# Performance work log

Hardware: AMD Instinct MI355X
Metric: run time of the kernel (lower is better)

The kernel has to match this reference:

```python
import jax, jax.numpy as jnp
import numpy as np
from jax import lax

B, TS, NN, FC = 16, 16, 4096, 1
HIDDEN = 64


def setup_inputs() -> dict:
    key = jax.random.key(0)
    k1, k2, k3, k4, k5 = jax.random.split(key, 5)
    x = jax.random.normal(k1, (B, TS, NN, FC), dtype=jnp.float32)
    # Conv2d(in_ch + hidden -> 4*hidden, kernel=3, padding=1), OIHW layout
    conv_w = jax.random.normal(k2, (4 * HIDDEN, FC + HIDDEN, 3, 3), dtype=jnp.float32) * 0.05
    conv_b = jax.random.normal(k3, (4 * HIDDEN,), dtype=jnp.float32) * 0.05
    # fc: Conv2d(hidden -> 1, kernel=1)
    fc_w = jax.random.normal(k4, (1, HIDDEN, 1, 1), dtype=jnp.float32) * 0.05
    fc_b = jax.random.normal(k5, (1,), dtype=jnp.float32) * 0.05
    return {"x": x, "conv_w": conv_w, "conv_b": conv_b, "fc_w": fc_w, "fc_b": fc_b}


def _convlstm_forward(x, conv_w, conv_b, fc_w, fc_b):
    Bb, Ts, Nn, Fc = x.shape
    hidden = fc_w.shape[1]
    # [B, Ts, Fc, Nn, 1] -> scan over time axis: [Ts, B, Fc, Nn, 1]
    xp = jnp.transpose(x, (0, 1, 3, 2))[..., None]
    xs = jnp.swapaxes(xp, 0, 1)
    h0 = jnp.zeros((Bb, hidden, Nn, 1), dtype=x.dtype)
    c0 = jnp.zeros_like(h0)

    dn = lax.conv_dimension_numbers(h0.shape[:1] + (Fc + hidden, Nn, 1), conv_w.shape, ("NCHW", "OIHW", "NCHW"))

    def step(carry, xt):
        h, c = carry
        inp = jnp.concatenate([xt, h], axis=1)  # [B, Fc+hidden, Nn, 1]
        gates = lax.conv_general_dilated(inp, conv_w, (1, 1), ((1, 1), (1, 1)), dimension_numbers=dn)
        gates = gates + conv_b[None, :, None, None]
        i, f, o, g = jnp.split(gates, 4, axis=1)
        c2 = jax.nn.sigmoid(f) * c + jax.nn.sigmoid(i) * jnp.tanh(g)
        h2 = jax.nn.sigmoid(o) * jnp.tanh(c2)
        return (h2, c2), None

    (h, c), _ = lax.scan(step, (h0, c0), xs)
    # fc: 1x1 conv -> [B, 1, Nn, 1]
    out = jnp.einsum("bchw,oc->bohw", h, fc_w[:, :, 0, 0]) + fc_b[None, :, None, None]
    out = out[..., 0]                 # [B, 1, Nn]
    out = jnp.transpose(out, (0, 2, 1))[:, None]  # [B, 1, Nn, 1]
    return jnp.broadcast_to(out, (Bb, Ts, Nn, 1))


def reference(x, conv_w, conv_b, fc_w, fc_b):
    return _convlstm_forward(x, conv_w, conv_b, fc_w, fc_b)
```

## Files before the change

kernel.cpp:

```cpp
#include <hip/hip_runtime.h>

typedef _Float16 f16;
typedef __attribute__((ext_vector_type(8))) _Float16 half8;
typedef __attribute__((ext_vector_type(4))) float floatx4;

#define BB    16
#define TSN   16
#define NNP   4096
#define HID   64
#define KPK   224
#define WOUT  128
#define HALO  8
#define WCMP  144
#define HROWS 146
#define NMS   9
#define NTIL  32

#define LOG2E 1.44269504088896340736f

__device__ __forceinline__ int hadr(int rr, int c) {
    return rr * 64 + ((c ^ (rr & 7)) << 3);
}
__device__ __forceinline__ unsigned f16pair(float a, float b) {
    union { f16 h; unsigned short u; } ua, ub;
    ua.h = (f16)a; ub.h = (f16)b;
    return (unsigned)ua.u | ((unsigned)ub.u << 16);
}
__device__ __forceinline__ unsigned pkrtz(float a, float b) {
    typedef __fp16 h2v __attribute__((ext_vector_type(2)));
    h2v r = __builtin_amdgcn_cvt_pkrtz(a, b);
    union { h2v h; unsigned u; } cv; cv.h = r; return cv.u;
}

__device__ __forceinline__ float fast_exp2(float x) {
#if __has_builtin(__builtin_amdgcn_exp2f)
    return __builtin_amdgcn_exp2f(x);
#else
    return exp2f(x);
#endif
}
__device__ __forceinline__ float fast_rcp(float x) {
#if __has_builtin(__builtin_amdgcn_rcpf)
    return __builtin_amdgcn_rcpf(x);
#else
    return 1.0f / x;
#endif
}

__device__ __forceinline__ float dpp_xor8(float v) {
    return __int_as_float(__builtin_amdgcn_mov_dpp(__float_as_int(v), 0x128, 0xF, 0xF, true));
}
__device__ __forceinline__ float dpp_xor1(float v) {
    return __int_as_float(__builtin_amdgcn_mov_dpp(__float_as_int(v), 0xB1, 0xF, 0xF, true));
}

__global__ void pack_w_kernel(const float* __restrict__ conv_w,
                              const float* __restrict__ conv_b,
                              f16* __restrict__ wpack) {
    int idx = blockIdx.x * 256 + threadIdx.x;
    if (idx >= 4 * 64 * KPK) return;
    int k  = idx % KPK;
    int oc = idx / KPK;
    int kt = k >> 5, c = k & 31;
    float w = 0.0f;
    if (kt < 6) {
        int tap = kt >> 1;
        int j   = (kt & 1) * 32 + c;
        w = conv_w[((oc * 65 + 1 + j) * 3 + tap) * 3 + 1];
    } else if (c < 3) {
        w = conv_w[((oc * 65 + 0) * 3 + c) * 3 + 1];
    } else if (c == 3) {
        w = conv_b[oc];
    }
    float scale = (oc >= 192) ? (2.0f * LOG2E) : (-LOG2E);
    wpack[oc * KPK + k] = (f16)(w * scale);
}

template <int MS>
__device__ __forceinline__ void do_mfma(
    const f16* __restrict__ hrd, const f16* __restrict__ xts,
    const half8 (&bf)[7][2], const floatx4& zacc,
    floatx4 (&acc)[2], int m, int kg)
{
    const int ar = MS * 16 + m;
    {
        half8 a = *(const half8*)(xts + ar * 8);
        acc[0] = __builtin_amdgcn_mfma_f32_16x16x32_f16(a, bf[6][0], zacc, 0, 0, 0);
        acc[1] = __builtin_amdgcn_mfma_f32_16x16x32_f16(a, bf[6][1], zacc, 0, 0, 0);
    }
#pragma unroll
    for (int kt = 0; kt < 6; ++kt) {
        half8 a = *(const half8*)(hrd + hadr(ar + (kt >> 1), (kt & 1) * 4 + kg));
        acc[0] = __builtin_amdgcn_mfma_f32_16x16x32_f16(a, bf[kt][0], acc[0], 0, 0, 0);
        acc[1] = __builtin_amdgcn_mfma_f32_16x16x32_f16(a, bf[kt][1], acc[1], 0, 0, 0);
    }
}

template <int MS>
__device__ __forceinline__ void do_epi(
    f16* __restrict__ hwr, floatx4 (&acc)[2], float (&creg)[NMS * 2],
    int m, int kg, int wave, bool lowm, bool edge, int n0)
{
    float pg[2][2];
#pragma unroll
    for (int q = 0; q < 2; ++q)
#pragma unroll
        for (int j = 0; j < 2; ++j) {
            float send = lowm ? acc[q][2 + j] : acc[q][j];
            pg[q][j] = dpp_xor8(send);
        }

#pragma unroll
    for (int j = 0; j < 2; ++j) {
        int r  = lowm ? j : 2 + j;
        float yi = lowm ? acc[0][j] : pg[0][j];
        float yf = lowm ? pg[0][j] : acc[0][2 + j];
        float yo = lowm ? acc[1][j] : pg[1][j];
        float yg = lowm ? pg[1][j] : acc[1][2 + j];
        float Ei = fast_exp2(yi);
        float Ef = fast_exp2(yf);
        float Eo = fast_exp2(yo);
        float Eg = fast_exp2(yg);
        float Fi = 1.0f + Ei, Ff = 1.0f + Ef, Fo = 1.0f + Eo, Fg = 1.0f + Eg;
        const int ridx = MS * 2 + j;
        float P  = Fi * Fg;
        float N  = fmaf(Eg - 1.0f, Ff, creg[ridx] * P);
        float cn = N * fast_rcp(P * Ff);
        float Ec = fast_exp2(cn * (2.0f * LOG2E));
        float hnf = (Ec - 1.0f) * fast_rcp(Fo * (1.0f + Ec));
        creg[ridx] = cn;
        int rit = MS * 16 + kg * 4 + r;
        if (edge) {
            int pos = n0 - HALO + rit;
            if (pos < 0 || pos >= NNP) hnf = 0.0f;
        }
        float po = dpp_xor1(hnf);
        if (!(m & 1)) {
            int rr = rit + 1;
            ((unsigned*)hwr)[rr * 32 + ((wave ^ (rr & 7)) << 2) + ((m & 7) >> 1)] =
                pkrtz(hnf, po);
        }
    }
}

__global__ __launch_bounds__(512, 2)
void lstm_kernel(const float* __restrict__ x, const f16* __restrict__ wpack,
                 f16* __restrict__ h_glob, float* __restrict__ c_glob, int phase)
{
    __shared__ __align__(16) f16 hlds[2][HROWS * 64];
    __shared__ __align__(16) f16 xt[8 * WCMP * 8];

    const int blk  = blockIdx.x;
    const int b    = blk >> 5;
    const int tau  = blk & 31;
    const int n0   = tau * WOUT;
    const int tid  = threadIdx.x;
    const int lane = tid & 63;
    const int wave = tid >> 6;
    const int m    = lane & 15;
    const int kg   = lane >> 4;
    const int gh   = m >> 3;
    const int hid  = wave * 8 + (m & 7);
    const bool lowm = (m < 8);
    const bool edge = (tau == 0) || (tau == NTIL - 1);
    const int s0   = phase * 8;

    half8 bf[7][2];
#pragma unroll
    for (int kt = 0; kt < 7; ++kt)
#pragma unroll
        for (int q = 0; q < 2; ++q)
            bf[kt][q] = *(const half8*)(wpack + (size_t)((q * 2 + gh) * 64 + hid) * KPK + kt * 32 + kg * 8);

    const floatx4 zacc = {0.0f, 0.0f, 0.0f, 0.0f};

    float creg[NMS * 2];

    for (int i = tid; i < 8 * WCMP; i += 512) {
        int ss = i / WCMP, r = i - ss * WCMP;
        const float* xb = x + ((size_t)b * TSN + s0 + ss) * NNP;
        int p = n0 - HALO + r;
        float v0 = (p - 1 >= 0 && p - 1 < NNP) ? xb[p - 1] : 0.0f;
        float v1 = (p >= 0 && p < NNP) ? xb[p] : 0.0f;
        float v2 = (p + 1 >= 0 && p + 1 < NNP) ? xb[p + 1] : 0.0f;
        unsigned* q = (unsigned*)(xt + (size_t)i * 8);
        q[0] = f16pair(v0, v1);
        q[1] = f16pair(v2, 1.0f);
        q[2] = 0u; q[3] = 0u;
    }

    if (phase == 0) {
#pragma unroll
        for (int i = 0; i < NMS * 2; ++i) creg[i] = 0.0f;
        for (int i = tid; i < HROWS * 64; i += 512) { hlds[0][i] = (f16)0; hlds[1][i] = (f16)0; }
    } else {
        for (int i = tid; i < HROWS * 8; i += 512) {
            int rr = i >> 3, c = i & 7;
            int pos = n0 - HALO - 1 + rr;
            half8 v = {};
            if (pos >= 0 && pos < NNP)
                v = *(const half8*)(h_glob + ((size_t)b * NNP + pos) * HID + c * 8);
            *(half8*)(hlds[0] + hadr(rr, c)) = v;
        }
        for (int i = tid; i < 2 * 64; i += 512) {
            int rr = (i >= 64) ? (HROWS - 1) : 0;
            hlds[1][rr * 64 + (i & 63)] = (f16)0;
        }
#pragma unroll
        for (int ms = 0; ms < NMS; ++ms)
#pragma unroll
            for (int j = 0; j < 2; ++j) {
                int r   = lowm ? j : 2 + j;
                int pos = n0 - HALO + ms * 16 + kg * 4 + r;
                creg[ms * 2 + j] = (pos >= 0 && pos < NNP)
                    ? c_glob[((size_t)b * NNP + pos) * HID + hid] : 0.0f;
            }
    }

#pragma unroll 1
    for (int s = s0; s < s0 + 8; ++s) {
        __syncthreads();
        const f16* hrd = hlds[s & 1];
        f16*       hwr = hlds[(s & 1) ^ 1];
        const f16* xts = xt + (size_t)(s - s0) * WCMP * 8;

        floatx4 accA[2], accB[2];
#define MF(MS, A)  do_mfma<MS>(hrd, xts, bf, zacc, A, m, kg)
#define EP(MS, A)  do_epi<MS>(hwr, A, creg, m, kg, wave, lowm, edge, n0)
        if (wave < 4) {
            MF(0, accA);
            MF(1, accB); EP(0, accA);
            MF(2, accA); EP(1, accB);
            MF(3, accB); EP(2, accA);
            MF(4, accA); EP(3, accB);
            MF(5, accB); EP(4, accA);
            MF(6, accA); EP(5, accB);
            MF(7, accB); EP(6, accA);
            MF(8, accA); EP(7, accB);
            EP(8, accA);
        } else {
            MF(4, accA);
            MF(5, accB); EP(4, accA);
            MF(6, accA); EP(5, accB);
            MF(7, accB); EP(6, accA);
            MF(8, accA); EP(7, accB);
            MF(0, accB); EP(8, accA);
            MF(1, accA); EP(0, accB);
            MF(2, accB); EP(1, accA);
            MF(3, accA); EP(2, accB);
            EP(3, accA);
        }
#undef MF
#undef EP
    }
    __syncthreads();

    for (int i = tid; i < WOUT * 8; i += 512) {
        int row = i >> 3, c = i & 7;
        half8 v = *(const half8*)(hlds[0] + hadr(row + HALO + 1, c));
        *(half8*)(h_glob + ((size_t)b * NNP + n0 + row) * HID + c * 8) = v;
    }
    if (phase == 0) {
#pragma unroll
        for (int ms = 0; ms < NMS; ++ms)
#pragma unroll
            for (int j = 0; j < 2; ++j) {
                int r   = lowm ? j : 2 + j;
                int rit = ms * 16 + kg * 4 + r;
                int pos = n0 - HALO + rit;
                if (rit >= HALO && rit < HALO + WOUT && pos >= 0 && pos < NNP)
                    c_glob[((size_t)b * NNP + pos) * HID + hid] = creg[ms * 2 + j];
            }
    }
}

__global__ void fc_kernel(const f16* __restrict__ h, const float* __restrict__ fc_w,
                          const float* __restrict__ fc_b, float* __restrict__ out) {
    int idx = blockIdx.x * 256 + threadIdx.x;
    const half8* hp = (const half8*)(h + (size_t)idx * HID);
    float s = 0.0f;
#pragma unroll
    for (int q = 0; q < 8; ++q) {
        half8 v = hp[q];
#pragma unroll
        for (int e = 0; e < 8; ++e) s += (float)v[e] * fc_w[q * 8 + e];
    }
    s += fc_b[0];
    int b = idx >> 12, n = idx & (NNP - 1);
#pragma unroll
    for (int t = 0; t < TSN; ++t) out[((size_t)b * TSN + t) * NNP + n] = s;
}

extern "C" void kernel_launch(void* const* d_in, const int* in_sizes, int n_in,
                              void* d_out, int out_size, void* d_ws, size_t ws_size,
                              hipStream_t stream) {
    const float* x      = (const float*)d_in[0];
    const float* conv_w = (const float*)d_in[1];
    const float* conv_b = (const float*)d_in[2];
    const float* fc_w   = (const float*)d_in[3];
    const float* fc_b   = (const float*)d_in[4];
    float* out = (float*)d_out;

    char* ws = (char*)d_ws;
    const size_t hbytes = (size_t)BB * NNP * HID * sizeof(f16);
    f16*   wpack  = (f16*)ws;
    f16*   h_glob = (f16*)(ws + 131072);
    float* c_glob = (float*)(ws + 131072 + hbytes);

    pack_w_kernel<<<(4 * 64 * KPK + 255) / 256, 256, 0, stream>>>(conv_w, conv_b, wpack);
    lstm_kernel<<<BB * NTIL, 512, 0, stream>>>(x, wpack, h_glob, c_glob, 0);
    lstm_kernel<<<BB * NTIL, 512, 0, stream>>>(x, wpack, h_glob, c_glob, 1);
    fc_kernel<<<BB * NNP / 256, 256, 0, stream>>>(h_glob, fc_w, fc_b, out);
}
```

Baseline: 250.0 us.

## Hoist x-input MFMAs before barrier, prioritize h MFMAs, batch exp2 in epilogue

Moves the input-only (x) MFMA for the first two tiles of each step ahead of the per-step barrier, so that work overlaps the synchronization wait. Raises wave priority around the recurrent-h MFMA chain, and groups the eight exp2 evaluations in the epilogue to expose more instruction-level parallelism. Also raises the launch-bounds minimum from 2 to 4 blocks, which tightens the register budget. The tighter register cap risks spills given the large creg and bf arrays held in registers.

Result: slower. 492.1 us (+96.8%).

```diff
diff --git a/kernel.cpp b/kernel.cpp
--- a/kernel.cpp
+++ b/kernel.cpp
@@ -77,23 +77,30 @@
 }
 
 template <int MS>
-__device__ __forceinline__ void do_mfma(
-    const f16* __restrict__ hrd, const f16* __restrict__ xts,
-    const half8 (&bf)[7][2], const floatx4& zacc,
+__device__ __forceinline__ void do_mfx(
+    const f16* __restrict__ xts, const half8 (&bf)[7][2],
+    const floatx4& zacc, floatx4 (&acc)[2], int m)
+{
+    const int ar = MS * 16 + m;
+    half8 a = *(const half8*)(xts + ar * 8);
+    acc[0] = __builtin_amdgcn_mfma_f32_16x16x32_f16(a, bf[6][0], zacc, 0, 0, 0);
+    acc[1] = __builtin_amdgcn_mfma_f32_16x16x32_f16(a, bf[6][1], zacc, 0, 0, 0);
+}
+
+template <int MS>
+__device__ __forceinline__ void do_mfh(
+    const f16* __restrict__ hrd, const half8 (&bf)[7][2],
     floatx4 (&acc)[2], int m, int kg)
 {
     const int ar = MS * 16 + m;
-    {
-        half8 a = *(const half8*)(xts + ar * 8);
-        acc[0] = __builtin_amdgcn_mfma_f32_16x16x32_f16(a, bf[6][0], zacc, 0, 0, 0);
-        acc[1] = __builtin_amdgcn_mfma_f32_16x16x32_f16(a, bf[6][1], zacc, 0, 0, 0);
-    }
+    __builtin_amdgcn_s_setprio(1);
 #pragma unroll
     for (int kt = 0; kt < 6; ++kt) {
         half8 a = *(const half8*)(hrd + hadr(ar + (kt >> 1), (kt & 1) * 4 + kg));
         acc[0] = __builtin_amdgcn_mfma_f32_16x16x32_f16(a, bf[kt][0], acc[0], 0, 0, 0);
         acc[1] = __builtin_amdgcn_mfma_f32_16x16x32_f16(a, bf[kt][1], acc[1], 0, 0, 0);
     }
+    __builtin_amdgcn_s_setprio(0);
 }
 
 template <int MS>
@@ -110,21 +117,28 @@
             pg[q][j] = dpp_xor8(send);
         }
 
+    float Y[2][4];
+#pragma unroll
+    for (int j = 0; j < 2; ++j) {
+        Y[j][0] = lowm ? acc[0][j] : pg[0][j];
+        Y[j][1] = lowm ? pg[0][j] : acc[0][2 + j];
+        Y[j][2] = lowm ? acc[1][j] : pg[1][j];
+        Y[j][3] = lowm ? pg[1][j] : acc[1][2 + j];
+    }
+    float E[2][4];
+#pragma unroll
+    for (int j = 0; j < 2; ++j)
+#pragma unroll
+        for (int g = 0; g < 4; ++g) E[j][g] = fast_exp2(Y[j][g]);
+
 #pragma unroll
     for (int j = 0; j < 2; ++j) {
         int r  = lowm ? j : 2 + j;
-        float yi = lowm ? acc[0][j] : pg[0][j];
-        float yf = lowm ? pg[0][j] : acc[0][2 + j];
-        float yo = lowm ? acc[1][j] : pg[1][j];
-        float yg = lowm ? pg[1][j] : acc[1][2 + j];
-        float Ei = fast_exp2(yi);
-        float Ef = fast_exp2(yf);
-        float Eo = fast_exp2(yo);
-        float Eg = fast_exp2(yg);
-        float Fi = 1.0f + Ei, Ff = 1.0f + Ef, Fo = 1.0f + Eo, Fg = 1.0f + Eg;
+        float Fi = 1.0f + E[j][0], Ff = 1.0f + E[j][1];
+        float Fo = 1.0f + E[j][2], Fg = 1.0f + E[j][3];
         const int ridx = MS * 2 + j;
         float P  = Fi * Fg;
-        float N  = fmaf(Eg - 1.0f, Ff, creg[ridx] * P);
+        float N  = fmaf(E[j][3] - 1.0f, Ff, creg[ridx] * P);
         float cn = N * fast_rcp(P * Ff);
         float Ec = fast_exp2(cn * (2.0f * LOG2E));
         float hnf = (Ec - 1.0f) * fast_rcp(Fo * (1.0f + Ec));
@@ -143,7 +157,7 @@
     }
 }
 
-__global__ __launch_bounds__(512, 2)
+__global__ __launch_bounds__(512, 4)
 void lstm_kernel(const float* __restrict__ x, const f16* __restrict__ wpack,
                  f16* __restrict__ h_glob, float* __restrict__ c_glob, int phase)
 {
@@ -217,40 +231,50 @@
             }
     }
 
+    __syncthreads();
+
 #pragma unroll 1
     for (int s = s0; s < s0 + 8; ++s) {
-        __syncthreads();
         const f16* hrd = hlds[s & 1];
         f16*       hwr = hlds[(s & 1) ^ 1];
         const f16* xts = xt + (size_t)(s - s0) * WCMP * 8;
 
         floatx4 accA[2], accB[2];
-#define MF(MS, A)  do_mfma<MS>(hrd, xts, bf, zacc, A, m, kg)
+#define MFX(MS, A) do_mfx<MS>(xts, bf, zacc, A, m)
+#define MFH(MS, A) do_mfh<MS>(hrd, bf, A, m, kg)
+#define MFF(MS, A) do { MFX(MS, A); MFH(MS, A); } while (0)
 #define EP(MS, A)  do_epi<MS>(hwr, A, creg, m, kg, wave, lowm, edge, n0)
+        if (wave < 4) { MFX(0, accA); MFX(1, accB); }
+        else          { MFX(4, accA); MFX(5, accB); }
+
+        __syncthreads();
+
         if (wave < 4) {
-            MF(0, accA);
-            MF(1, accB); EP(0, accA);
-            MF(2, accA); EP(1, accB);
-            MF(3, accB); EP(2, accA);
-            MF(4, accA); EP(3, accB);
-            MF(5, accB); EP(4, accA);
-            MF(6, accA); EP(5, accB);
-            MF(7, accB); EP(6, accA);
-            MF(8, accA); EP(7, accB);
+            MFH(0, accA);
+            MFH(1, accB); EP(0, accA);
+            MFF(2, accA); EP(1, accB);
+            MFF(3, accB); EP(2, accA);
+            MFF(4, accA); EP(3, accB);
+            MFF(5, accB); EP(4, accA);
+            MFF(6, accA); EP(5, accB);
+            MFF(7, accB); EP(6, accA);
+            MFF(8, accA); EP(7, accB);
             EP(8, accA);
         } else {
-            MF(4, accA);
-            MF(5, accB); EP(4, accA);
-            MF(6, accA); EP(5, accB);
-            MF(7, accB); EP(6, accA);
-            MF(8, accA); EP(7, accB);
-            MF(0, accB); EP(8, accA);
-            MF(1, accA); EP(0, accB);
-            MF(2, accB); EP(1, accA);
-            MF(3, accA); EP(2, accB);
+            MFH(4, accA);
+            MFH(5, accB); EP(4, accA);
+            MFF(6, accA); EP(5, accB);
+            MFF(7, accB); EP(6, accA);
+            MFF(8, accA); EP(7, accB);
+            MFF(0, accB); EP(8, accA);
+            MFF(1, accA); EP(0, accB);
+            MFF(2, accB); EP(1, accA);
+            MFF(3, accA); EP(2, accB);
             EP(3, accA);
         }
-#undef MF
+#undef MFX
+#undef MFH
+#undef MFF
 #undef EP
     }
     __syncthreads();
```
